# Kernel tuning notes

Hardware: AMD Instinct MI355X
Metric: run time of the kernel (lower is better)

## Reference

```python
import jax, jax.numpy as jnp
import numpy as np

LN_EPS = 1e-5


def setup_inputs() -> dict:
    key = jax.random.key(0)
    ks = jax.random.split(key, 8)
    N, c_z, H, C = 256, 128, 4, 32
    s = 0.02  # small init scale for stable softmax
    return {
        "z": jax.random.normal(ks[0], (N, N, c_z), dtype=jnp.float32),
        "ln_g": jnp.ones((c_z,), jnp.float32),
        "ln_b": jnp.zeros((c_z,), jnp.float32),
        "Wb": jax.random.normal(ks[1], (c_z, H), dtype=jnp.float32) * s,
        "Wq": jax.random.normal(ks[2], (c_z, H, C), dtype=jnp.float32) * s,
        "Wk": jax.random.normal(ks[3], (c_z, H, C), dtype=jnp.float32) * s,
        "Wv": jax.random.normal(ks[4], (c_z, H, C), dtype=jnp.float32) * s,
        "Wg": jax.random.normal(ks[5], (c_z, H, C), dtype=jnp.float32) * s,
        "bg": jnp.ones((H, C), jnp.float32),
        "Wo": jax.random.normal(ks[6], (H, C, c_z), dtype=jnp.float32) * s,
        "bo": jnp.zeros((c_z,), jnp.float32),
    }


def reference(z, ln_g, ln_b, Wb, Wq, Wk, Wv, Wg, bg, Wo, bo):
    # TriangleAttention, node_type='starting_node' (Algorithm 13).
    # z: (N, N, c_z)
    C = Wq.shape[-1]
    # LayerNorm over c_z
    mu = jnp.mean(z, axis=-1, keepdims=True)
    var = jnp.var(z, axis=-1, keepdims=True)
    x = (z - mu) * jax.lax.rsqrt(var + LN_EPS) * ln_g + ln_b
    # pairwise additive bias: b[h, j, k] = (x @ Wb)[j, k, h]
    b = jnp.einsum('jkz,zh->hjk', x, Wb)
    # per-head projections; attention over second residue axis (-2),
    # first residue axis i acts as batch
    q = jnp.einsum('ijz,zhc->ijhc', x, Wq)
    k = jnp.einsum('ijz,zhc->ijhc', x, Wk)
    v = jnp.einsum('ijz,zhc->ijhc', x, Wv)
    scores = jnp.einsum('iqhc,ikhc->hiqk', q, k) / jnp.sqrt(jnp.asarray(C, x.dtype))
    scores = scores + b[:, None, :, :]  # broadcast bias over batch axis i
    a = jax.nn.softmax(scores, axis=-1)  # (h, i, q, k)
    o = jnp.einsum('hiqk,ikhc->iqhc', a, v)
    g = jax.nn.sigmoid(jnp.einsum('ijz,zhc->ijhc', x, Wg) + bg)
    o = o * g
    out = jnp.einsum('iqhc,hcz->iqz', o, Wo) + bo
    return out
```

## Files before the change

kernel.cpp:

```cpp
#include <hip/hip_runtime.h>
#include <hip/hip_bf16.h>
#include <math.h>


#define NN 256
#define CZ 128
#define NHEAD 4
#define CH 32

typedef __attribute__((ext_vector_type(8))) short bf16x8;
typedef __attribute__((ext_vector_type(4))) float f32x4;

__device__ __forceinline__ f32x4 mfma16(bf16x8 a, bf16x8 b, f32x4 c) {
  return __builtin_amdgcn_mfma_f32_16x16x32_bf16(a, b, c, 0, 0, 0);
}
__device__ __forceinline__ unsigned short f2bf(float f) {
  unsigned b = __float_as_uint(f);
  return (unsigned short)((b + 0x7FFFu + ((b >> 16) & 1u)) >> 16);
}
__device__ __forceinline__ float bf2f(unsigned short u) { return __uint_as_float((unsigned)u << 16); }

__global__ __launch_bounds__(128) void k_prep(const float* __restrict__ Wq, const float* __restrict__ Wk,
                                              const float* __restrict__ Wv, const float* __restrict__ Wg,
                                              const float* __restrict__ Wo, unsigned short* __restrict__ Wt) {
  int n = blockIdx.x, t = threadIdx.x;
  const float* srcs[5] = {Wq, Wk, Wv, Wg, Wo};
  float v = srcs[n >> 7][t * 128 + (n & 127)];
  Wt[n * 128 + t] = f2bf(v);
}

__global__ __launch_bounds__(256) void k_ln(const float* __restrict__ z,
                                            const float* __restrict__ ln_g,
                                            const float* __restrict__ ln_b,
                                            const float* __restrict__ Wb,
                                            unsigned short* __restrict__ xb,
                                            float* __restrict__ bT) {
  int wave = threadIdx.x >> 6, lane = threadIdx.x & 63;
  int pos = blockIdx.x * 4 + wave;
  float2 v = ((const float2*)(z + (size_t)pos * CZ))[lane];
  float s = v.x + v.y, sq = v.x * v.x + v.y * v.y;
#pragma unroll
  for (int o = 1; o < 64; o <<= 1) { s += __shfl_xor(s, o); sq += __shfl_xor(sq, o); }
  float mean = s * (1.0f / CZ);
  float var = sq * (1.0f / CZ) - mean * mean;
  float rstd = rsqrtf(var + 1e-5f);
  int c0 = lane * 2;
  float x0 = (v.x - mean) * rstd * ln_g[c0] + ln_b[c0];
  float x1 = (v.y - mean) * rstd * ln_g[c0 + 1] + ln_b[c0 + 1];
  unsigned pk = (unsigned)f2bf(x0) | ((unsigned)f2bf(x1) << 16);
  ((unsigned*)(xb + (size_t)pos * CZ))[lane] = pk;
  float4 w0 = *(const float4*)(Wb + c0 * NHEAD);
  float4 w1 = *(const float4*)(Wb + (c0 + 1) * NHEAD);
  float b0 = x0 * w0.x + x1 * w1.x;
  float b1 = x0 * w0.y + x1 * w1.y;
  float b2 = x0 * w0.z + x1 * w1.z;
  float b3 = x0 * w0.w + x1 * w1.w;
#pragma unroll
  for (int o = 1; o < 64; o <<= 1) {
    b0 += __shfl_xor(b0, o); b1 += __shfl_xor(b1, o);
    b2 += __shfl_xor(b2, o); b3 += __shfl_xor(b3, o);
  }
  if (lane == 0) {
    int j = pos >> 8, kk = pos & 255;
    bT[0 * 65536 + kk * 256 + j] = b0;
    bT[1 * 65536 + kk * 256 + j] = b1;
    bT[2 * 65536 + kk * 256 + j] = b2;
    bT[3 * 65536 + kk * 256 + j] = b3;
  }
}

__global__ __launch_bounds__(256) void k_proj(const unsigned short* __restrict__ xb,
                                              const unsigned short* __restrict__ Wt,
                                              const float* __restrict__ bg,
                                              unsigned short* __restrict__ qw,
                                              unsigned short* __restrict__ kw,
                                              unsigned short* __restrict__ vT,
                                              unsigned short* __restrict__ gw) {
  int t = threadIdx.x, w = t >> 6, lane = t & 63;
  int l16 = lane & 15, g = lane >> 4;
  int wr = w >> 1, wc = w & 1;
  int sec = blockIdx.y;
  int pbase = blockIdx.x * 128 + wr * 64;
  int cbase = wc * 64;
  f32x4 acc[4][4];
#pragma unroll
  for (int m = 0; m < 4; m++)
#pragma unroll
    for (int n = 0; n < 4; n++) acc[m][n] = (f32x4){0.f, 0.f, 0.f, 0.f};
#pragma unroll
  for (int kt = 0; kt < 4; kt++) {
    bf16x8 a[4], b[4];
#pragma unroll
    for (int m = 0; m < 4; m++)
      a[m] = *(const bf16x8*)(xb + (size_t)(pbase + m * 16 + l16) * CZ + kt * 32 + g * 8);
#pragma unroll
    for (int n = 0; n < 4; n++)
      b[n] = *(const bf16x8*)(Wt + (size_t)(sec * 128 + cbase + n * 16 + l16) * CZ + kt * 32 + g * 8);
#pragma unroll
    for (int m = 0; m < 4; m++)
#pragma unroll
      for (int n = 0; n < 4; n++) acc[m][n] = mfma16(a[m], b[n], acc[m][n]);
  }
  if (sec == 0 || sec == 3) {
    unsigned short* dst = (sec == 0) ? qw : gw;
#pragma unroll
    for (int n = 0; n < 4; n++) {
      int hc = cbase + n * 16 + l16;
      float bgv = (sec == 3) ? bg[hc] : 0.0f;
#pragma unroll
      for (int m = 0; m < 4; m++) {
#pragma unroll
        for (int r = 0; r < 4; r++) {
          int p = pbase + m * 16 + g * 4 + r;
          float v = acc[m][n][r];
          if (sec == 3) v = 1.0f / (1.0f + __expf(-(v + bgv)));
          dst[(size_t)p * 128 + hc] = f2bf(v);
        }
      }
    }
  } else if (sec == 1) {
#pragma unroll
    for (int n = 0; n < 4; n++) {
      int hc = cbase + n * 16 + l16;
      int h = hc >> 5, c = hc & 31;
#pragma unroll
      for (int m = 0; m < 4; m++) {
        int p0 = pbase + m * 16 + g * 4;
        int i = p0 >> 8, j = p0 & 255;
        size_t base = ((size_t)(i * NHEAD + h) * 256 + j) * CH + c;
#pragma unroll
        for (int r = 0; r < 4; r++) kw[base + (size_t)r * CH] = f2bf(acc[m][n][r]);
      }
    }
  } else {
#pragma unroll
    for (int n = 0; n < 4; n++) {
      int hc = cbase + n * 16 + l16;
      int h = hc >> 5, c = hc & 31;
#pragma unroll
      for (int m = 0; m < 4; m++) {
        int p0 = pbase + m * 16 + g * 4;
        int i = p0 >> 8, j = p0 & 255;
        ushort4 pk;
        pk.x = f2bf(acc[m][n][0]); pk.y = f2bf(acc[m][n][1]);
        pk.z = f2bf(acc[m][n][2]); pk.w = f2bf(acc[m][n][3]);
        *(ushort4*)(vT + (size_t)((i * NHEAD + h) * CH + c) * 256 + j) = pk;
      }
    }
  }
}

__global__ __launch_bounds__(256) void k_attn(const unsigned short* qw,
                                              const unsigned short* __restrict__ kw,
                                              const unsigned short* __restrict__ vT,
                                              const unsigned short* __restrict__ gw,
                                              const float* __restrict__ bT,
                                              unsigned short* ow ) {
  __shared__ unsigned short Ps[4][64][40];
  int i = blockIdx.x, h = blockIdx.y;
  int t = threadIdx.x, w = t >> 6, lane = t & 63, l16 = lane & 15, g = lane >> 4;
  int qbase = w * 64;
  bf16x8 qa[4];
#pragma unroll
  for (int m = 0; m < 4; m++)
    qa[m] = *(const bf16x8*)(qw + (size_t)(i * 256 + qbase + m * 16 + l16) * 128 + h * 32 + g * 8);
  f32x4 o[4][2], lsum[4];
#pragma unroll
  for (int m = 0; m < 4; m++) {
    lsum[m] = (f32x4){0.f, 0.f, 0.f, 0.f};
#pragma unroll
    for (int n = 0; n < 2; n++) o[m][n] = (f32x4){0.f, 0.f, 0.f, 0.f};
  }
  const unsigned short* kb_base = kw + (size_t)(i * NHEAD + h) * 256 * CH;
  const unsigned short* vb_base = vT + (size_t)(i * NHEAD + h) * CH * 256;
  const float* bb = bT + (size_t)h * 65536;
  const float sc = 0.17677669529663687f;
  for (int kc = 0; kc < 8; kc++) {
    bf16x8 kb[2];
#pragma unroll
    for (int n = 0; n < 2; n++)
      kb[n] = *(const bf16x8*)(kb_base + (size_t)(kc * 32 + n * 16 + l16) * CH + g * 8);
#pragma unroll
    for (int m = 0; m < 4; m++) {
#pragma unroll
      for (int n = 0; n < 2; n++) {
        f32x4 s = mfma16(qa[m], kb[n], (f32x4){0.f, 0.f, 0.f, 0.f});
        float4 bv = *(const float4*)(bb + (size_t)(kc * 32 + n * 16 + l16) * 256 + qbase + m * 16 + g * 4);
        f32x4 p;
        p[0] = __expf(s[0] * sc + bv.x);
        p[1] = __expf(s[1] * sc + bv.y);
        p[2] = __expf(s[2] * sc + bv.z);
        p[3] = __expf(s[3] * sc + bv.w);
        lsum[m] += p;
#pragma unroll
        for (int r = 0; r < 4; r++) Ps[w][m * 16 + g * 4 + r][n * 16 + l16] = f2bf(p[r]);
      }
    }
    bf16x8 vb[2];
#pragma unroll
    for (int n = 0; n < 2; n++)
      vb[n] = *(const bf16x8*)(vb_base + (size_t)(n * 16 + l16) * 256 + kc * 32 + g * 8);
#pragma unroll
    for (int m = 0; m < 4; m++) {
      bf16x8 pa = *(const bf16x8*)(&Ps[w][m * 16 + l16][g * 8]);
#pragma unroll
      for (int n = 0; n < 2; n++) o[m][n] = mfma16(pa, vb[n], o[m][n]);
    }
  }
#pragma unroll
  for (int m = 0; m < 4; m++)
#pragma unroll
    for (int off = 1; off < 16; off <<= 1)
#pragma unroll
      for (int r = 0; r < 4; r++) lsum[m][r] += __shfl_xor(lsum[m][r], off);
#pragma unroll
  for (int m = 0; m < 4; m++) {
    f32x4 inv;
#pragma unroll
    for (int r = 0; r < 4; r++) inv[r] = 1.0f / lsum[m][r];
#pragma unroll
    for (int n = 0; n < 2; n++) {
#pragma unroll
      for (int r = 0; r < 4; r++) {
        int q = qbase + m * 16 + g * 4 + r;
        size_t idx = (size_t)(i * 256 + q) * 128 + h * 32 + n * 16 + l16;
        float gv = bf2f(gw[idx]);
        ow[idx] = f2bf(o[m][n][r] * inv[r] * gv);
      }
    }
  }
}

__global__ __launch_bounds__(256) void k_out(const unsigned short* __restrict__ og,
                                             const unsigned short* __restrict__ WoT,
                                             const float* __restrict__ bo,
                                             float* __restrict__ out) {
  int t = threadIdx.x, w = t >> 6, lane = t & 63, l16 = lane & 15, g = lane >> 4;
  int wr = w >> 1, wc = w & 1;
  int pbase = blockIdx.x * 128 + wr * 64;
  int cbase = wc * 64;
  f32x4 acc[4][4];
#pragma unroll
  for (int m = 0; m < 4; m++)
#pragma unroll
    for (int n = 0; n < 4; n++) acc[m][n] = (f32x4){0.f, 0.f, 0.f, 0.f};
#pragma unroll
  for (int kt = 0; kt < 4; kt++) {
    bf16x8 a[4], b[4];
#pragma unroll
    for (int m = 0; m < 4; m++)
      a[m] = *(const bf16x8*)(og + (size_t)(pbase + m * 16 + l16) * 128 + kt * 32 + g * 8);
#pragma unroll
    for (int n = 0; n < 4; n++)
      b[n] = *(const bf16x8*)(WoT + (size_t)(cbase + n * 16 + l16) * 128 + kt * 32 + g * 8);
#pragma unroll
    for (int m = 0; m < 4; m++)
#pragma unroll
      for (int n = 0; n < 4; n++) acc[m][n] = mfma16(a[m], b[n], acc[m][n]);
  }
#pragma unroll
  for (int n = 0; n < 4; n++) {
    int zc = cbase + n * 16 + l16;
    float bv = bo[zc];
#pragma unroll
    for (int m = 0; m < 4; m++) {
#pragma unroll
      for (int r = 0; r < 4; r++)
        out[(size_t)(pbase + m * 16 + g * 4 + r) * 128 + zc] = acc[m][n][r] + bv;
    }
  }
}

extern "C" void kernel_launch(void* const* d_in, const int* in_sizes, int n_in,
                              void* d_out, int out_size, void* d_ws, size_t ws_size,
                              hipStream_t stream) {
  const float* z    = (const float*)d_in[0];
  const float* ln_g = (const float*)d_in[1];
  const float* ln_b = (const float*)d_in[2];
  const float* Wb   = (const float*)d_in[3];
  const float* Wq   = (const float*)d_in[4];
  const float* Wk   = (const float*)d_in[5];
  const float* Wv   = (const float*)d_in[6];
  const float* Wg   = (const float*)d_in[7];
  const float* bg   = (const float*)d_in[8];
  const float* Wo   = (const float*)d_in[9];
  const float* bo   = (const float*)d_in[10];
  float* out = (float*)d_out;

  char* ws = (char*)d_ws;
  unsigned short* xb = (unsigned short*)(ws + 0);
  float*          bT = (float*)(ws + 16777216);
  unsigned short* qw = (unsigned short*)(ws + 17825792);
  unsigned short* kw = (unsigned short*)(ws + 34603008);
  unsigned short* vT = (unsigned short*)(ws + 51380224);
  unsigned short* gw = (unsigned short*)(ws + 68157440);
  unsigned short* Wt = (unsigned short*)(ws + 84934656);

  k_prep<<<640, 128, 0, stream>>>(Wq, Wk, Wv, Wg, Wo, Wt);
  k_ln<<<16384, 256, 0, stream>>>(z, ln_g, ln_b, Wb, xb, bT);
  k_proj<<<dim3(512, 4), 256, 0, stream>>>(xb, Wt, bg, qw, kw, vT, gw);
  k_attn<<<dim3(256, 4), 256, 0, stream>>>(qw, kw, vT, gw, bT, qw);
  k_out<<<512, 256, 0, stream>>>(qw, Wt + 512 * 128, bo, out);
}
```

Measured before the change: 225.1 us.

## Fuse projection, attention, gating and output projection into one per-row kernel

Replaces the separate projection, attention and output kernels with one kernel per batch row i. It computes K/V/Q/G for each head into shared memory, runs the attention, applies the gate and accumulates the output projection in registers. This removes the round trips of q, k, v, g and the gated output through global memory, plus two launches. In exchange only 256 blocks of 512 threads run with launch_bounds(512,1), which lowers parallelism and occupancy, and the heads are processed serially with extra barriers.

```diff
diff --git a/kernel.cpp b/kernel.cpp
--- a/kernel.cpp
+++ b/kernel.cpp
@@ -5,8 +5,6 @@
 
 #define NN 256
 #define CZ 128
-#define NHEAD 4
-#define CH 32
 
 typedef __attribute__((ext_vector_type(8))) short bf16x8;
 typedef __attribute__((ext_vector_type(4))) float f32x4;
@@ -18,7 +16,6 @@
   unsigned b = __float_as_uint(f);
   return (unsigned short)((b + 0x7FFFu + ((b >> 16) & 1u)) >> 16);
 }
-__device__ __forceinline__ float bf2f(unsigned short u) { return __uint_as_float((unsigned)u << 16); }
 
 __global__ __launch_bounds__(128) void k_prep(const float* __restrict__ Wq, const float* __restrict__ Wk,
                                               const float* __restrict__ Wv, const float* __restrict__ Wg,
@@ -49,8 +46,8 @@
   float x1 = (v.y - mean) * rstd * ln_g[c0 + 1] + ln_b[c0 + 1];
   unsigned pk = (unsigned)f2bf(x0) | ((unsigned)f2bf(x1) << 16);
   ((unsigned*)(xb + (size_t)pos * CZ))[lane] = pk;
-  float4 w0 = *(const float4*)(Wb + c0 * NHEAD);
-  float4 w1 = *(const float4*)(Wb + (c0 + 1) * NHEAD);
+  float4 w0 = *(const float4*)(Wb + c0 * 4);
+  float4 w1 = *(const float4*)(Wb + (c0 + 1) * 4);
   float b0 = x0 * w0.x + x1 * w1.x;
   float b1 = x0 * w0.y + x1 * w1.y;
   float b2 = x0 * w0.z + x1 * w1.z;
@@ -69,205 +66,196 @@
   }
 }
 
-__global__ __launch_bounds__(256) void k_proj(const unsigned short* __restrict__ xb,
-                                              const unsigned short* __restrict__ Wt,
-                                              const float* __restrict__ bg,
-                                              unsigned short* __restrict__ qw,
-                                              unsigned short* __restrict__ kw,
-                                              unsigned short* __restrict__ vT,
-                                              unsigned short* __restrict__ gw) {
-  int t = threadIdx.x, w = t >> 6, lane = t & 63;
-  int l16 = lane & 15, g = lane >> 4;
-  int wr = w >> 1, wc = w & 1;
-  int sec = blockIdx.y;
-  int pbase = blockIdx.x * 128 + wr * 64;
-  int cbase = wc * 64;
-  f32x4 acc[4][4];
-#pragma unroll
-  for (int m = 0; m < 4; m++)
-#pragma unroll
-    for (int n = 0; n < 4; n++) acc[m][n] = (f32x4){0.f, 0.f, 0.f, 0.f};
-#pragma unroll
-  for (int kt = 0; kt < 4; kt++) {
-    bf16x8 a[4], b[4];
-#pragma unroll
-    for (int m = 0; m < 4; m++)
-      a[m] = *(const bf16x8*)(xb + (size_t)(pbase + m * 16 + l16) * CZ + kt * 32 + g * 8);
-#pragma unroll
-    for (int n = 0; n < 4; n++)
-      b[n] = *(const bf16x8*)(Wt + (size_t)(sec * 128 + cbase + n * 16 + l16) * CZ + kt * 32 + g * 8);
-#pragma unroll
-    for (int m = 0; m < 4; m++)
-#pragma unroll
-      for (int n = 0; n < 4; n++) acc[m][n] = mfma16(a[m], b[n], acc[m][n]);
-  }
-  if (sec == 0 || sec == 3) {
-    unsigned short* dst = (sec == 0) ? qw : gw;
-#pragma unroll
-    for (int n = 0; n < 4; n++) {
-      int hc = cbase + n * 16 + l16;
-      float bgv = (sec == 3) ? bg[hc] : 0.0f;
-#pragma unroll
-      for (int m = 0; m < 4; m++) {
-#pragma unroll
-        for (int r = 0; r < 4; r++) {
-          int p = pbase + m * 16 + g * 4 + r;
-          float v = acc[m][n][r];
-          if (sec == 3) v = 1.0f / (1.0f + __expf(-(v + bgv)));
-          dst[(size_t)p * 128 + hc] = f2bf(v);
+__global__ __launch_bounds__(512, 1) void k_fused(const unsigned short* __restrict__ xb,
+                                                  const unsigned short* __restrict__ Wt,
+                                                  const float* __restrict__ bT,
+                                                  const float* __restrict__ bg,
+                                                  const float* __restrict__ bo,
+                                                  float* __restrict__ out) {
+  __shared__ unsigned short ks[256][40];
+  __shared__ unsigned short vt[32][264];
+  __shared__ unsigned short qs[8][32][40];
+  int i = blockIdx.x;
+  int t = threadIdx.x, w = t >> 6, lane = t & 63, l16 = lane & 15, g = lane >> 4;
+  int rbase = w * 32;
+  const float sc = 0.17677669529663687f;
+
+  bf16x8 xa[2][4];
+#pragma unroll
+  for (int m = 0; m < 2; m++)
+#pragma unroll
+    for (int kt = 0; kt < 4; kt++)
+      xa[m][kt] = *(const bf16x8*)(xb + (size_t)(i * 256 + rbase + m * 16 + l16) * CZ + kt * 32 + g * 8);
+
+  f32x4 oac[2][8];
+#pragma unroll
+  for (int m = 0; m < 2; m++)
+#pragma unroll
+    for (int n = 0; n < 8; n++) oac[m][n] = (f32x4){0.f, 0.f, 0.f, 0.f};
+
+  for (int h = 0; h < 4; h++) {
+    __syncthreads();
+    f32x4 d[2][2];
+#pragma unroll
+    for (int m = 0; m < 2; m++)
+#pragma unroll
+      for (int n = 0; n < 2; n++) d[m][n] = (f32x4){0.f, 0.f, 0.f, 0.f};
+#pragma unroll
+    for (int kt = 0; kt < 4; kt++)
+#pragma unroll
+      for (int n = 0; n < 2; n++) {
+        bf16x8 b = *(const bf16x8*)(Wt + (size_t)(128 + h * 32 + n * 16 + l16) * CZ + kt * 32 + g * 8);
+#pragma unroll
+        for (int m = 0; m < 2; m++) d[m][n] = mfma16(xa[m][kt], b, d[m][n]);
+      }
+#pragma unroll
+    for (int m = 0; m < 2; m++)
+#pragma unroll
+      for (int n = 0; n < 2; n++)
+#pragma unroll
+        for (int r = 0; r < 4; r++) ks[rbase + m * 16 + g * 4 + r][n * 16 + l16] = f2bf(d[m][n][r]);
+#pragma unroll
+    for (int m = 0; m < 2; m++)
+#pragma unroll
+      for (int n = 0; n < 2; n++) d[m][n] = (f32x4){0.f, 0.f, 0.f, 0.f};
+#pragma unroll
+    for (int kt = 0; kt < 4; kt++)
+#pragma unroll
+      for (int n = 0; n < 2; n++) {
+        bf16x8 b = *(const bf16x8*)(Wt + (size_t)(256 + h * 32 + n * 16 + l16) * CZ + kt * 32 + g * 8);
+#pragma unroll
+        for (int m = 0; m < 2; m++) d[m][n] = mfma16(xa[m][kt], b, d[m][n]);
+      }
+#pragma unroll
+    for (int m = 0; m < 2; m++)
+#pragma unroll
+      for (int n = 0; n < 2; n++) {
+        ushort4 pk;
+        pk.x = f2bf(d[m][n][0]); pk.y = f2bf(d[m][n][1]);
+        pk.z = f2bf(d[m][n][2]); pk.w = f2bf(d[m][n][3]);
+        *(ushort4*)&vt[n * 16 + l16][rbase + m * 16 + g * 4] = pk;
+      }
+#pragma unroll
+    for (int m = 0; m < 2; m++)
+#pragma unroll
+      for (int n = 0; n < 2; n++) d[m][n] = (f32x4){0.f, 0.f, 0.f, 0.f};
+#pragma unroll
+    for (int kt = 0; kt < 4; kt++)
+#pragma unroll
+      for (int n = 0; n < 2; n++) {
+        bf16x8 b = *(const bf16x8*)(Wt + (size_t)(0 + h * 32 + n * 16 + l16) * CZ + kt * 32 + g * 8);
+#pragma unroll
+        for (int m = 0; m < 2; m++) d[m][n] = mfma16(xa[m][kt], b, d[m][n]);
+      }
+#pragma unroll
+    for (int m = 0; m < 2; m++)
+#pragma unroll
+      for (int n = 0; n < 2; n++)
+#pragma unroll
+        for (int r = 0; r < 4; r++) qs[w][m * 16 + g * 4 + r][n * 16 + l16] = f2bf(d[m][n][r]);
+#pragma unroll
+    for (int m = 0; m < 2; m++)
+#pragma unroll
+      for (int n = 0; n < 2; n++) d[m][n] = (f32x4){0.f, 0.f, 0.f, 0.f};
+#pragma unroll
+    for (int kt = 0; kt < 4; kt++)
+#pragma unroll
+      for (int n = 0; n < 2; n++) {
+        bf16x8 b = *(const bf16x8*)(Wt + (size_t)(384 + h * 32 + n * 16 + l16) * CZ + kt * 32 + g * 8);
+#pragma unroll
+        for (int m = 0; m < 2; m++) d[m][n] = mfma16(xa[m][kt], b, d[m][n]);
+      }
+    float gt[2][2][4];
+    float bgv0 = bg[h * 32 + l16], bgv1 = bg[h * 32 + 16 + l16];
+#pragma unroll
+    for (int m = 0; m < 2; m++)
+#pragma unroll
+      for (int n = 0; n < 2; n++)
+#pragma unroll
+        for (int r = 0; r < 4; r++)
+          gt[m][n][r] = 1.0f / (1.0f + __expf(-(d[m][n][r] + (n ? bgv1 : bgv0))));
+    __syncthreads();
+
+    bf16x8 qa[2];
+#pragma unroll
+    for (int m = 0; m < 2; m++) qa[m] = *(const bf16x8*)&qs[w][m * 16 + l16][g * 8];
+    f32x4 oat[2][2], lsum[2];
+#pragma unroll
+    for (int m = 0; m < 2; m++) {
+      lsum[m] = (f32x4){0.f, 0.f, 0.f, 0.f};
+#pragma unroll
+      for (int n = 0; n < 2; n++) oat[m][n] = (f32x4){0.f, 0.f, 0.f, 0.f};
+    }
+    const float* bb = bT + (size_t)h * 65536;
+    for (int kc = 0; kc < 8; kc++) {
+      bf16x8 kb[2];
+#pragma unroll
+      for (int n = 0; n < 2; n++) kb[n] = *(const bf16x8*)&ks[kc * 32 + n * 16 + l16][g * 8];
+      f32x4 p[2][2];
+#pragma unroll
+      for (int m = 0; m < 2; m++)
+#pragma unroll
+        for (int n = 0; n < 2; n++) {
+          f32x4 s = mfma16(qa[m], kb[n], (f32x4){0.f, 0.f, 0.f, 0.f});
+          float4 bv = *(const float4*)(bb + (size_t)(kc * 32 + n * 16 + l16) * 256 + rbase + m * 16 + g * 4);
+          p[m][n][0] = __expf(s[0] * sc + bv.x);
+          p[m][n][1] = __expf(s[1] * sc + bv.y);
+          p[m][n][2] = __expf(s[2] * sc + bv.z);
+          p[m][n][3] = __expf(s[3] * sc + bv.w);
+          lsum[m] += p[m][n];
         }
-      }
-    }
-  } else if (sec == 1) {
-#pragma unroll
-    for (int n = 0; n < 4; n++) {
-      int hc = cbase + n * 16 + l16;
-      int h = hc >> 5, c = hc & 31;
-#pragma unroll
-      for (int m = 0; m < 4; m++) {
-        int p0 = pbase + m * 16 + g * 4;
-        int i = p0 >> 8, j = p0 & 255;
-        size_t base = ((size_t)(i * NHEAD + h) * 256 + j) * CH + c;
-#pragma unroll
-        for (int r = 0; r < 4; r++) kw[base + (size_t)r * CH] = f2bf(acc[m][n][r]);
-      }
-    }
-  } else {
-#pragma unroll
-    for (int n = 0; n < 4; n++) {
-      int hc = cbase + n * 16 + l16;
-      int h = hc >> 5, c = hc & 31;
-#pragma unroll
-      for (int m = 0; m < 4; m++) {
-        int p0 = pbase + m * 16 + g * 4;
-        int i = p0 >> 8, j = p0 & 255;
-        ushort4 pk;
-        pk.x = f2bf(acc[m][n][0]); pk.y = f2bf(acc[m][n][1]);
-        pk.z = f2bf(acc[m][n][2]); pk.w = f2bf(acc[m][n][3]);
-        *(ushort4*)(vT + (size_t)((i * NHEAD + h) * CH + c) * 256 + j) = pk;
-      }
-    }
-  }
-}
-
-__global__ __launch_bounds__(256) void k_attn(const unsigned short* qw,
-                                              const unsigned short* __restrict__ kw,
-                                              const unsigned short* __restrict__ vT,
-                                              const unsigned short* __restrict__ gw,
-                                              const float* __restrict__ bT,
-                                              unsigned short* ow ) {
-  __shared__ unsigned short Ps[4][64][40];
-  int i = blockIdx.x, h = blockIdx.y;
-  int t = threadIdx.x, w = t >> 6, lane = t & 63, l16 = lane & 15, g = lane >> 4;
-  int qbase = w * 64;
-  bf16x8 qa[4];
-#pragma unroll
-  for (int m = 0; m < 4; m++)
-    qa[m] = *(const bf16x8*)(qw + (size_t)(i * 256 + qbase + m * 16 + l16) * 128 + h * 32 + g * 8);
-  f32x4 o[4][2], lsum[4];
-#pragma unroll
-  for (int m = 0; m < 4; m++) {
-    lsum[m] = (f32x4){0.f, 0.f, 0.f, 0.f};
-#pragma unroll
-    for (int n = 0; n < 2; n++) o[m][n] = (f32x4){0.f, 0.f, 0.f, 0.f};
-  }
-  const unsigned short* kb_base = kw + (size_t)(i * NHEAD + h) * 256 * CH;
-  const unsigned short* vb_base = vT + (size_t)(i * NHEAD + h) * CH * 256;
-  const float* bb = bT + (size_t)h * 65536;
-  const float sc = 0.17677669529663687f;
-  for (int kc = 0; kc < 8; kc++) {
-    bf16x8 kb[2];
-#pragma unroll
-    for (int n = 0; n < 2; n++)
-      kb[n] = *(const bf16x8*)(kb_base + (size_t)(kc * 32 + n * 16 + l16) * CH + g * 8);
-#pragma unroll
-    for (int m = 0; m < 4; m++) {
-#pragma unroll
-      for (int n = 0; n < 2; n++) {
-        f32x4 s = mfma16(qa[m], kb[n], (f32x4){0.f, 0.f, 0.f, 0.f});
-        float4 bv = *(const float4*)(bb + (size_t)(kc * 32 + n * 16 + l16) * 256 + qbase + m * 16 + g * 4);
-        f32x4 p;
-        p[0] = __expf(s[0] * sc + bv.x);
-        p[1] = __expf(s[1] * sc + bv.y);
-        p[2] = __expf(s[2] * sc + bv.z);
-        p[3] = __expf(s[3] * sc + bv.w);
-        lsum[m] += p;
-#pragma unroll
-        for (int r = 0; r < 4; r++) Ps[w][m * 16 + g * 4 + r][n * 16 + l16] = f2bf(p[r]);
-      }
-    }
-    bf16x8 vb[2];
-#pragma unroll
-    for (int n = 0; n < 2; n++)
-      vb[n] = *(const bf16x8*)(vb_base + (size_t)(n * 16 + l16) * 256 + kc * 32 + g * 8);
-#pragma unroll
-    for (int m = 0; m < 4; m++) {
-      bf16x8 pa = *(const bf16x8*)(&Ps[w][m * 16 + l16][g * 8]);
-#pragma unroll
-      for (int n = 0; n < 2; n++) o[m][n] = mfma16(pa, vb[n], o[m][n]);
-    }
-  }
-#pragma unroll
-  for (int m = 0; m < 4; m++)
-#pragma unroll
-    for (int off = 1; off < 16; off <<= 1)
-#pragma unroll
-      for (int r = 0; r < 4; r++) lsum[m][r] += __shfl_xor(lsum[m][r], off);
-#pragma unroll
-  for (int m = 0; m < 4; m++) {
-    f32x4 inv;
-#pragma unroll
-    for (int r = 0; r < 4; r++) inv[r] = 1.0f / lsum[m][r];
-#pragma unroll
-    for (int n = 0; n < 2; n++) {
-#pragma unroll
-      for (int r = 0; r < 4; r++) {
-        int q = qbase + m * 16 + g * 4 + r;
-        size_t idx = (size_t)(i * 256 + q) * 128 + h * 32 + n * 16 + l16;
-        float gv = bf2f(gw[idx]);
-        ow[idx] = f2bf(o[m][n][r] * inv[r] * gv);
-      }
-    }
-  }
-}
-
-__global__ __launch_bounds__(256) void k_out(const unsigned short* __restrict__ og,
-                                             const unsigned short* __restrict__ WoT,
-                                             const float* __restrict__ bo,
-                                             float* __restrict__ out) {
-  int t = threadIdx.x, w = t >> 6, lane = t & 63, l16 = lane & 15, g = lane >> 4;
-  int wr = w >> 1, wc = w & 1;
-  int pbase = blockIdx.x * 128 + wr * 64;
-  int cbase = wc * 64;
-  f32x4 acc[4][4];
-#pragma unroll
-  for (int m = 0; m < 4; m++)
-#pragma unroll
-    for (int n = 0; n < 4; n++) acc[m][n] = (f32x4){0.f, 0.f, 0.f, 0.f};
-#pragma unroll
-  for (int kt = 0; kt < 4; kt++) {
-    bf16x8 a[4], b[4];
-#pragma unroll
-    for (int m = 0; m < 4; m++)
-      a[m] = *(const bf16x8*)(og + (size_t)(pbase + m * 16 + l16) * 128 + kt * 32 + g * 8);
-#pragma unroll
-    for (int n = 0; n < 4; n++)
-      b[n] = *(const bf16x8*)(WoT + (size_t)(cbase + n * 16 + l16) * 128 + kt * 32 + g * 8);
-#pragma unroll
-    for (int m = 0; m < 4; m++)
-#pragma unroll
-      for (int n = 0; n < 4; n++) acc[m][n] = mfma16(a[m], b[n], acc[m][n]);
-  }
-#pragma unroll
-  for (int n = 0; n < 4; n++) {
-    int zc = cbase + n * 16 + l16;
+#pragma unroll
+      for (int m = 0; m < 2; m++)
+#pragma unroll
+        for (int n = 0; n < 2; n++)
+#pragma unroll
+          for (int r = 0; r < 4; r++) qs[w][m * 16 + g * 4 + r][n * 16 + l16] = f2bf(p[m][n][r]);
+      bf16x8 pa[2], vb[2];
+#pragma unroll
+      for (int m = 0; m < 2; m++) pa[m] = *(const bf16x8*)&qs[w][m * 16 + l16][g * 8];
+#pragma unroll
+      for (int n = 0; n < 2; n++) vb[n] = *(const bf16x8*)&vt[n * 16 + l16][kc * 32 + g * 8];
+#pragma unroll
+      for (int m = 0; m < 2; m++)
+#pragma unroll
+        for (int n = 0; n < 2; n++) oat[m][n] = mfma16(pa[m], vb[n], oat[m][n]);
+    }
+#pragma unroll
+    for (int m = 0; m < 2; m++)
+#pragma unroll
+      for (int off = 1; off < 16; off <<= 1)
+#pragma unroll
+        for (int r = 0; r < 4; r++) lsum[m][r] += __shfl_xor(lsum[m][r], off);
+#pragma unroll
+    for (int m = 0; m < 2; m++) {
+      f32x4 inv;
+#pragma unroll
+      for (int r = 0; r < 4; r++) inv[r] = 1.0f / lsum[m][r];
+#pragma unroll
+      for (int n = 0; n < 2; n++)
+#pragma unroll
+        for (int r = 0; r < 4; r++)
+          qs[w][m * 16 + g * 4 + r][n * 16 + l16] = f2bf(oat[m][n][r] * inv[r] * gt[m][n][r]);
+    }
+    bf16x8 pa2[2];
+#pragma unroll
+    for (int m = 0; m < 2; m++) pa2[m] = *(const bf16x8*)&qs[w][m * 16 + l16][g * 8];
+#pragma unroll
+    for (int n2 = 0; n2 < 8; n2++) {
+      bf16x8 wb = *(const bf16x8*)(Wt + (size_t)(512 + n2 * 16 + l16) * CZ + h * 32 + g * 8);
+#pragma unroll
+      for (int m = 0; m < 2; m++) oac[m][n2] = mfma16(pa2[m], wb, oac[m][n2]);
+    }
+  }
+#pragma unroll
+  for (int n2 = 0; n2 < 8; n2++) {
+    int zc = n2 * 16 + l16;
     float bv = bo[zc];
 #pragma unroll
-    for (int m = 0; m < 4; m++) {
+    for (int m = 0; m < 2; m++)
 #pragma unroll
       for (int r = 0; r < 4; r++)
-        out[(size_t)(pbase + m * 16 + g * 4 + r) * 128 + zc] = acc[m][n][r] + bv;
-    }
+        out[(size_t)(i * 256 + rbase + m * 16 + g * 4 + r) * 128 + zc] = oac[m][n2][r] + bv;
   }
 }
 
@@ -290,15 +278,9 @@
   char* ws = (char*)d_ws;
   unsigned short* xb = (unsigned short*)(ws + 0);
   float*          bT = (float*)(ws + 16777216);
-  unsigned short* qw = (unsigned short*)(ws + 17825792);
-  unsigned short* kw = (unsigned short*)(ws + 34603008);
-  unsigned short* vT = (unsigned short*)(ws + 51380224);
-  unsigned short* gw = (unsigned short*)(ws + 68157440);
-  unsigned short* Wt = (unsigned short*)(ws + 84934656);
+  unsigned short* Wt = (unsigned short*)(ws + 17825792);
 
   k_prep<<<640, 128, 0, stream>>>(Wq, Wk, Wv, Wg, Wo, Wt);
   k_ln<<<16384, 256, 0, stream>>>(z, ln_g, ln_b, Wb, xb, bT);
-  k_proj<<<dim3(512, 4), 256, 0, stream>>>(xb, Wt, bg, qw, kw, vT, gw);
-  k_attn<<<dim3(256, 4), 256, 0, stream>>>(qw, kw, vT, gw, bT, qw);
-  k_out<<<512, 256, 0, stream>>>(qw, Wt + 512 * 128, bo, out);
-}
+  k_fused<<<256, 512, 0, stream>>>(xb, Wt, bT, bg, bo, out);
+}
```

Measured after the change: 217.1 us. 1.04x faster.
